# Kernel tuning notes

Hardware: AMD Instinct MI355X
Metric: run time of the kernel (lower is better)

The kernel has to match this reference:

```python
import jax, jax.numpy as jnp
import numpy as np

EPS = 1e-08


def setup_inputs() -> dict:
    key = jax.random.key(0)
    student_output = jax.random.normal(key, (8192, 1024), dtype=jnp.float32)
    return {"student_output": student_output}


def reference(student_output) -> jnp.ndarray:
    # F.normalize(p=2, dim=-1, eps=EPS): x / max(||x||_2, eps)
    x = student_output.astype(jnp.float32)
    norm = jnp.linalg.norm(x, axis=-1, keepdims=True)
    x = x / jnp.maximum(norm, EPS)

    n = x.shape[0]
    # full similarity matrix with diagonal masked to -1.0 (self-sim excluded)
    sim = x @ x.T  # [N, N]
    sim = jnp.where(jnp.eye(n, dtype=bool), jnp.float32(-1.0), sim)
    indices = jnp.argmax(sim, axis=1)  # nearest neighbor per row

    # torch.nn.PairwiseDistance(2, eps): ||x1 - x2 + eps||_2 along feature dim
    diff = x - x[indices] + EPS
    distances = jnp.sqrt(jnp.sum(diff * diff, axis=-1))

    return -jnp.mean(jnp.log(distances + EPS))
```

## Files before the change

### kernel.cpp

```cpp
#include <hip/hip_runtime.h>
#include <stdint.h>

#define N 8192
#define DIM 1024
#define EPSF 1e-8f
#define NBLK 32
#define NTRI 528

typedef __attribute__((ext_vector_type(4))) float f32x4;
typedef __attribute__((ext_vector_type(8))) short s16x8;

__device__ inline unsigned short f2bf(float f) {
  unsigned u = __float_as_uint(f);
  unsigned r = (u + 0x7FFFu + ((u >> 16) & 1u)) >> 16;
  return (unsigned short)r;
}

__device__ inline unsigned encf(float f) {
  unsigned u = __float_as_uint(f);
  return (u & 0x80000000u) ? ~u : (u | 0x80000000u);
}

#define XB_OFF   0
#define INV_OFF  16777216
#define KEY_OFF  16809984
#define PART_OFF 16875520

__global__ __launch_bounds__(256)
void k_norm(const float* __restrict__ x, unsigned short* __restrict__ xb,
            float* __restrict__ invn, unsigned long long* __restrict__ keys) {
  int row = blockIdx.x, t = threadIdx.x;
  const float4* xr = (const float4*)(x + (size_t)row * DIM);
  float4 v = xr[t];
  float ss = v.x * v.x + v.y * v.y + v.z * v.z + v.w * v.w;
#pragma unroll
  for (int o = 32; o > 0; o >>= 1) ss += __shfl_down(ss, o, 64);
  __shared__ float red[4];
  __shared__ float sinv;
  if ((t & 63) == 0) red[t >> 6] = ss;
  __syncthreads();
  if (t == 0) {
    float s = red[0] + red[1] + red[2] + red[3];
    float inv = 1.0f / fmaxf(sqrtf(s), EPSF);
    sinv = inv;
    invn[row] = inv;
    keys[row] = 0ull;
  }
  __syncthreads();
  float inv = sinv;
  ushort4 o4;
  o4.x = f2bf(v.x * inv);
  o4.y = f2bf(v.y * inv);
  o4.z = f2bf(v.z * inv);
  o4.w = f2bf(v.w * inv);
  ((ushort4*)(xb + (size_t)row * DIM))[t] = o4;
}

__global__ __launch_bounds__(512, 2)
void k_sim(const unsigned short* __restrict__ xb, unsigned long long* __restrict__ keys) {
  int b = blockIdx.x;
  int bi = (int)((65.0f - sqrtf(4225.0f - 8.0f * (float)b)) * 0.5f);
  while ((bi + 1) * (65 - (bi + 1)) / 2 <= b) ++bi;
  while (bi * (65 - bi) / 2 > b) --bi;
  int bj = bi + (b - bi * (65 - bi) / 2);

  __shared__ unsigned short sA[2][8192];
  __shared__ unsigned short sB[2][8192];

  const int t = threadIdx.x, lane = t & 63, wv = t >> 6;
  const int wr = wv >> 2, wc = wv & 3;
  const int hi = lane >> 4, lo = lane & 15;
  const int rowBase = bi * 256, colBase = bj * 256;

  const unsigned short* gA = xb + (size_t)rowBase * DIM;
  const unsigned short* gB = xb + (size_t)colBase * DIM;

  const int sg = (lane & 3) ^ ((lane >> 3) & 3);
  const int r0 = wv * 16 + (lane >> 2);
  const size_t so0 = (size_t)r0 * DIM + sg * 8;
  const size_t so1 = (size_t)(r0 + 128) * DIM + sg * 8;
  const int lb0 = wv * 512;
  const int lb1 = 4096 + wv * 512;

  const f32x4 fzero = {0.f, 0.f, 0.f, 0.f};
  f32x4 acc[8][4];
#pragma unroll
  for (int i = 0; i < 8; ++i)
#pragma unroll
    for (int j = 0; j < 4; ++j) acc[i][j] = fzero;

  const int sr8 = (hi ^ ((lo >> 1) & 3)) * 8;

  __builtin_amdgcn_global_load_lds((const __attribute__((address_space(1))) void*)(gA + so0),
                                   (__attribute__((address_space(3))) void*)(&sA[0][lb0]), 16, 0, 0);
  __builtin_amdgcn_global_load_lds((const __attribute__((address_space(1))) void*)(gA + so1),
                                   (__attribute__((address_space(3))) void*)(&sA[0][lb1]), 16, 0, 0);
  __builtin_amdgcn_global_load_lds((const __attribute__((address_space(1))) void*)(gB + so0),
                                   (__attribute__((address_space(3))) void*)(&sB[0][lb0]), 16, 0, 0);
  __builtin_amdgcn_global_load_lds((const __attribute__((address_space(1))) void*)(gB + so1),
                                   (__attribute__((address_space(3))) void*)(&sB[0][lb1]), 16, 0, 0);
  asm volatile("s_waitcnt vmcnt(0)" ::: "memory");
  __builtin_amdgcn_s_barrier();

  for (int kt = 0; kt < 32; ++kt) {
    const int cur = kt & 1, nxt = cur ^ 1;
    const size_t ko = (size_t)(kt + 1) * 32;
    s16x8 af[4], bf[4];

    if (kt < 31) {
      __builtin_amdgcn_global_load_lds((const __attribute__((address_space(1))) void*)(gA + so0 + ko),
                                       (__attribute__((address_space(3))) void*)(&sA[nxt][lb0]), 16, 0, 0);
      __builtin_amdgcn_global_load_lds((const __attribute__((address_space(1))) void*)(gA + so1 + ko),
                                       (__attribute__((address_space(3))) void*)(&sA[nxt][lb1]), 16, 0, 0);
    }
#pragma unroll
    for (int mi = 0; mi < 4; ++mi) {
      int r = wr * 128 + mi * 16 + lo;
      af[mi] = *(const s16x8*)(&sA[cur][r * 32 + sr8]);
    }
#pragma unroll
    for (int ni = 0; ni < 4; ++ni) {
      int r = wc * 64 + ni * 16 + lo;
      bf[ni] = *(const s16x8*)(&sB[cur][r * 32 + sr8]);
    }
    __builtin_amdgcn_s_barrier();
    __builtin_amdgcn_s_setprio(1);
#pragma unroll
    for (int mi = 0; mi < 4; ++mi)
#pragma unroll
      for (int ni = 0; ni < 4; ++ni)
        acc[mi][ni] = __builtin_amdgcn_mfma_f32_16x16x32_bf16(af[mi], bf[ni], acc[mi][ni], 0, 0, 0);
    __builtin_amdgcn_s_setprio(0);
    __builtin_amdgcn_s_barrier();

    if (kt < 31) {
      __builtin_amdgcn_global_load_lds((const __attribute__((address_space(1))) void*)(gB + so0 + ko),
                                       (__attribute__((address_space(3))) void*)(&sB[nxt][lb0]), 16, 0, 0);
      __builtin_amdgcn_global_load_lds((const __attribute__((address_space(1))) void*)(gB + so1 + ko),
                                       (__attribute__((address_space(3))) void*)(&sB[nxt][lb1]), 16, 0, 0);
    }
#pragma unroll
    for (int mi = 0; mi < 4; ++mi) {
      int r = wr * 128 + 64 + mi * 16 + lo;
      af[mi] = *(const s16x8*)(&sA[cur][r * 32 + sr8]);
    }
    __builtin_amdgcn_s_barrier();
    __builtin_amdgcn_s_setprio(1);
#pragma unroll
    for (int mi = 0; mi < 4; ++mi)
#pragma unroll
      for (int ni = 0; ni < 4; ++ni)
        acc[4 + mi][ni] = __builtin_amdgcn_mfma_f32_16x16x32_bf16(af[mi], bf[ni], acc[4 + mi][ni], 0, 0, 0);
    __builtin_amdgcn_s_setprio(0);
    asm volatile("s_waitcnt vmcnt(0)" ::: "memory");
    __builtin_amdgcn_s_barrier();
  }

#pragma unroll
  for (int am = 0; am < 8; ++am) {
#pragma unroll
    for (int reg = 0; reg < 4; ++reg) {
      int grow = rowBase + wr * 128 + am * 16 + hi * 4 + reg;
      float best = -10.0f;
      int bcol = 0;
#pragma unroll
      for (int ni = 0; ni < 4; ++ni) {
        int gcol = colBase + wc * 64 + ni * 16 + lo;
        float v = acc[am][ni][reg];
        v = (gcol == grow) ? -10.0f : v;
        if (v > best || (v == best && gcol < bcol)) { best = v; bcol = gcol; }
      }
#pragma unroll
      for (int m = 1; m < 16; m <<= 1) {
        float ov = __shfl_xor(best, m, 64);
        int oc = __shfl_xor(bcol, m, 64);
        if (ov > best || (ov == best && oc < bcol)) { best = ov; bcol = oc; }
      }
      if (lo == 0) {
        unsigned long long key = ((unsigned long long)encf(best) << 32) | (unsigned)(~bcol);
        atomicMax(&keys[grow], key);
      }
    }
  }

  if (bi != bj) {
#pragma unroll
    for (int ni = 0; ni < 4; ++ni) {
      int gcol = colBase + wc * 64 + ni * 16 + lo;
      float best = -10.0f;
      int brow = 0;
#pragma unroll
      for (int am = 0; am < 8; ++am)
#pragma unroll
        for (int reg = 0; reg < 4; ++reg) {
          int grow = rowBase + wr * 128 + am * 16 + hi * 4 + reg;
          float v = acc[am][ni][reg];
          if (v > best || (v == best && grow < brow)) { best = v; brow = grow; }
        }
#pragma unroll
      for (int m = 16; m < 64; m <<= 1) {
        float ov = __shfl_xor(best, m, 64);
        int oc = __shfl_xor(brow, m, 64);
        if (ov > best || (ov == best && oc < brow)) { best = ov; brow = oc; }
      }
      if (hi == 0) {
        unsigned long long key = ((unsigned long long)encf(best) << 32) | (unsigned)(~brow);
        atomicMax(&keys[gcol], key);
      }
    }
  }
}

__global__ __launch_bounds__(256)
void k_dist(const float* __restrict__ x, const float* __restrict__ invn,
            const unsigned long long* __restrict__ keys, float* __restrict__ part) {
  int row = blockIdx.x, t = threadIdx.x;
  unsigned long long key = keys[row];
  int nb = (int)(~(unsigned)key);
  float ia = invn[row], ib = invn[nb];
  float4 a = ((const float4*)(x + (size_t)row * DIM))[t];
  float4 b = ((const float4*)(x + (size_t)nb * DIM))[t];
  float d0 = a.x * ia - b.x * ib + EPSF;
  float d1 = a.y * ia - b.y * ib + EPSF;
  float d2 = a.z * ia - b.z * ib + EPSF;
  float d3 = a.w * ia - b.w * ib + EPSF;
  float ss = d0 * d0 + d1 * d1 + d2 * d2 + d3 * d3;
#pragma unroll
  for (int o = 32; o > 0; o >>= 1) ss += __shfl_down(ss, o, 64);
  __shared__ float red[4];
  if ((t & 63) == 0) red[t >> 6] = ss;
  __syncthreads();
  if (t == 0) {
    float s = red[0] + red[1] + red[2] + red[3];
    part[row] = logf(sqrtf(s) + EPSF);
  }
}

__global__ __launch_bounds__(1024)
void k_final(const float* __restrict__ part, float* __restrict__ out) {
  int t = threadIdx.x;
  float s = 0.0f;
#pragma unroll
  for (int i = 0; i < N / 1024; ++i) s += part[t + i * 1024];
#pragma unroll
  for (int o = 32; o > 0; o >>= 1) s += __shfl_down(s, o, 64);
  __shared__ float red[16];
  if ((t & 63) == 0) red[t >> 6] = s;
  __syncthreads();
  if (t == 0) {
    float tot = 0.0f;
#pragma unroll
    for (int i = 0; i < 16; ++i) tot += red[i];
    out[0] = -tot / (float)N;
  }
}

extern "C" void kernel_launch(void* const* d_in, const int* in_sizes, int n_in,
                              void* d_out, int out_size, void* d_ws, size_t ws_size,
                              hipStream_t stream) {
  const float* x = (const float*)d_in[0];
  float* out = (float*)d_out;
  char* ws = (char*)d_ws;
  unsigned short* xb = (unsigned short*)(ws + XB_OFF);
  float* invn = (float*)(ws + INV_OFF);
  unsigned long long* keys = (unsigned long long*)(ws + KEY_OFF);
  float* part = (float*)(ws + PART_OFF);

  k_norm<<<N, 256, 0, stream>>>(x, xb, invn, keys);
  k_sim<<<NTRI, 512, 0, stream>>>(xb, keys);
  k_dist<<<N, 256, 0, stream>>>(x, invn, keys, part);
  k_final<<<1, 1024, 0, stream>>>(part, out);
}
```

Before: 279.3 us.

## Use a four-stage LDS ring buffer with three tiles prefetched in k_sim

```diff
diff --git a/kernel.cpp b/kernel.cpp
--- a/kernel.cpp
+++ b/kernel.cpp
@@ -6,6 +6,7 @@
 #define EPSF 1e-8f
 #define NBLK 32
 #define NTRI 528
+#define NKT 32
 
 typedef __attribute__((ext_vector_type(4))) float f32x4;
 typedef __attribute__((ext_vector_type(8))) short s16x8;
@@ -58,15 +59,14 @@
 
 __global__ __launch_bounds__(512, 2)
 void k_sim(const unsigned short* __restrict__ xb, unsigned long long* __restrict__ keys) {
+  extern __shared__ unsigned short lds_us[];
+
   int b = blockIdx.x;
   int bi = (int)((65.0f - sqrtf(4225.0f - 8.0f * (float)b)) * 0.5f);
   while ((bi + 1) * (65 - (bi + 1)) / 2 <= b) ++bi;
   while (bi * (65 - bi) / 2 > b) --bi;
   int bj = bi + (b - bi * (65 - bi) / 2);
 
-  __shared__ unsigned short sA[2][8192];
-  __shared__ unsigned short sB[2][8192];
-
   const int t = threadIdx.x, lane = t & 63, wv = t >> 6;
   const int wr = wv >> 2, wc = wv & 3;
   const int hi = lane >> 4, lo = lane & 15;
@@ -76,11 +76,28 @@
   const unsigned short* gB = xb + (size_t)colBase * DIM;
 
   const int sg = (lane & 3) ^ ((lane >> 3) & 3);
-  const int r0 = wv * 16 + (lane >> 2);
-  const size_t so0 = (size_t)r0 * DIM + sg * 8;
-  const size_t so1 = (size_t)(r0 + 128) * DIM + sg * 8;
-  const int lb0 = wv * 512;
-  const int lb1 = 4096 + wv * 512;
+  const size_t soA0 = (size_t)(wv * 16 + (lane >> 2)) * DIM + sg * 8;
+  const size_t soA1 = soA0 + (size_t)128 * DIM;
+  const int ldsA0 = wv * 512;
+  const int ldsA1 = 4096 + wv * 512;
+
+#define STAGE_TILE(tt) do {                                                          \
+    const size_t ko_ = (size_t)(tt) * 32;                                            \
+    unsigned short* Ab_ = lds_us + ((tt) & 3) * 8192;                                \
+    unsigned short* Bb_ = lds_us + 32768 + ((tt) & 3) * 8192;                        \
+    __builtin_amdgcn_global_load_lds(                                                \
+        (const __attribute__((address_space(1))) void*)(gA + soA0 + ko_),            \
+        (__attribute__((address_space(3))) void*)(Ab_ + ldsA0), 16, 0, 0);           \
+    __builtin_amdgcn_global_load_lds(                                                \
+        (const __attribute__((address_space(1))) void*)(gA + soA1 + ko_),            \
+        (__attribute__((address_space(3))) void*)(Ab_ + ldsA1), 16, 0, 0);           \
+    __builtin_amdgcn_global_load_lds(                                                \
+        (const __attribute__((address_space(1))) void*)(gB + soA0 + ko_),            \
+        (__attribute__((address_space(3))) void*)(Bb_ + ldsA0), 16, 0, 0);           \
+    __builtin_amdgcn_global_load_lds(                                                \
+        (const __attribute__((address_space(1))) void*)(gB + soA1 + ko_),            \
+        (__attribute__((address_space(3))) void*)(Bb_ + ldsA1), 16, 0, 0);           \
+  } while (0)
 
   const f32x4 fzero = {0.f, 0.f, 0.f, 0.f};
   f32x4 acc[8][4];
@@ -89,72 +106,44 @@
 #pragma unroll
     for (int j = 0; j < 4; ++j) acc[i][j] = fzero;
 
-  const int sr8 = (hi ^ ((lo >> 1) & 3)) * 8;
-
-  __builtin_amdgcn_global_load_lds((const __attribute__((address_space(1))) void*)(gA + so0),
-                                   (__attribute__((address_space(3))) void*)(&sA[0][lb0]), 16, 0, 0);
-  __builtin_amdgcn_global_load_lds((const __attribute__((address_space(1))) void*)(gA + so1),
-                                   (__attribute__((address_space(3))) void*)(&sA[0][lb1]), 16, 0, 0);
-  __builtin_amdgcn_global_load_lds((const __attribute__((address_space(1))) void*)(gB + so0),
-                                   (__attribute__((address_space(3))) void*)(&sB[0][lb0]), 16, 0, 0);
-  __builtin_amdgcn_global_load_lds((const __attribute__((address_space(1))) void*)(gB + so1),
-                                   (__attribute__((address_space(3))) void*)(&sB[0][lb1]), 16, 0, 0);
-  asm volatile("s_waitcnt vmcnt(0)" ::: "memory");
-  __builtin_amdgcn_s_barrier();
-
-  for (int kt = 0; kt < 32; ++kt) {
-    const int cur = kt & 1, nxt = cur ^ 1;
-    const size_t ko = (size_t)(kt + 1) * 32;
-    s16x8 af[4], bf[4];
-
-    if (kt < 31) {
-      __builtin_amdgcn_global_load_lds((const __attribute__((address_space(1))) void*)(gA + so0 + ko),
-                                       (__attribute__((address_space(3))) void*)(&sA[nxt][lb0]), 16, 0, 0);
-      __builtin_amdgcn_global_load_lds((const __attribute__((address_space(1))) void*)(gA + so1 + ko),
-                                       (__attribute__((address_space(3))) void*)(&sA[nxt][lb1]), 16, 0, 0);
-    }
-#pragma unroll
-    for (int mi = 0; mi < 4; ++mi) {
+  const int chux = (hi ^ ((lo >> 1) & 3)) * 8;
+
+  STAGE_TILE(0);
+  STAGE_TILE(1);
+  STAGE_TILE(2);
+  asm volatile("s_waitcnt vmcnt(8)" ::: "memory");
+  asm volatile("s_barrier" ::: "memory");
+
+  for (int kt = 0; kt < NKT; ++kt) {
+    if (kt < NKT - 3) STAGE_TILE(kt + 3);
+
+    const unsigned short* Ab = lds_us + (kt & 3) * 8192;
+    const unsigned short* Bb = lds_us + 32768 + (kt & 3) * 8192;
+    s16x8 af[8], bfr[4];
+#pragma unroll
+    for (int mi = 0; mi < 8; ++mi) {
       int r = wr * 128 + mi * 16 + lo;
-      af[mi] = *(const s16x8*)(&sA[cur][r * 32 + sr8]);
+      af[mi] = *(const s16x8*)(Ab + r * 32 + chux);
     }
 #pragma unroll
     for (int ni = 0; ni < 4; ++ni) {
       int r = wc * 64 + ni * 16 + lo;
-      bf[ni] = *(const s16x8*)(&sB[cur][r * 32 + sr8]);
-    }
-    __builtin_amdgcn_s_barrier();
+      bfr[ni] = *(const s16x8*)(Bb + r * 32 + chux);
+    }
+
     __builtin_amdgcn_s_setprio(1);
 #pragma unroll
-    for (int mi = 0; mi < 4; ++mi)
+    for (int mi = 0; mi < 8; ++mi)
 #pragma unroll
       for (int ni = 0; ni < 4; ++ni)
-        acc[mi][ni] = __builtin_amdgcn_mfma_f32_16x16x32_bf16(af[mi], bf[ni], acc[mi][ni], 0, 0, 0);
+        acc[mi][ni] = __builtin_amdgcn_mfma_f32_16x16x32_bf16(af[mi], bfr[ni], acc[mi][ni], 0, 0, 0);
     __builtin_amdgcn_s_setprio(0);
-    __builtin_amdgcn_s_barrier();
-
-    if (kt < 31) {
-      __builtin_amdgcn_global_load_lds((const __attribute__((address_space(1))) void*)(gB + so0 + ko),
-                                       (__attribute__((address_space(3))) void*)(&sB[nxt][lb0]), 16, 0, 0);
-      __builtin_amdgcn_global_load_lds((const __attribute__((address_space(1))) void*)(gB + so1 + ko),
-                                       (__attribute__((address_space(3))) void*)(&sB[nxt][lb1]), 16, 0, 0);
-    }
-#pragma unroll
-    for (int mi = 0; mi < 4; ++mi) {
-      int r = wr * 128 + 64 + mi * 16 + lo;
-      af[mi] = *(const s16x8*)(&sA[cur][r * 32 + sr8]);
-    }
-    __builtin_amdgcn_s_barrier();
-    __builtin_amdgcn_s_setprio(1);
-#pragma unroll
-    for (int mi = 0; mi < 4; ++mi)
-#pragma unroll
-      for (int ni = 0; ni < 4; ++ni)
-        acc[4 + mi][ni] = __builtin_amdgcn_mfma_f32_16x16x32_bf16(af[mi], bf[ni], acc[4 + mi][ni], 0, 0, 0);
-    __builtin_amdgcn_s_setprio(0);
-    asm volatile("s_waitcnt vmcnt(0)" ::: "memory");
-    __builtin_amdgcn_s_barrier();
-  }
+
+    if (kt < NKT - 3) asm volatile("s_waitcnt vmcnt(8)" ::: "memory");
+    else              asm volatile("s_waitcnt vmcnt(0)" ::: "memory");
+    asm volatile("s_barrier" ::: "memory");
+  }
+#undef STAGE_TILE
 
 #pragma unroll
   for (int am = 0; am < 8; ++am) {
@@ -266,8 +255,11 @@
   unsigned long long* keys = (unsigned long long*)(ws + KEY_OFF);
   float* part = (float*)(ws + PART_OFF);
 
+  (void)hipFuncSetAttribute((const void*)k_sim,
+                            hipFuncAttributeMaxDynamicSharedMemorySize, 131072);
+
   k_norm<<<N, 256, 0, stream>>>(x, xb, invn, keys);
-  k_sim<<<NTRI, 512, 0, stream>>>(xb, keys);
+  k_sim<<<NTRI, 512, 131072, stream>>>(xb, keys);
   k_dist<<<N, 256, 0, stream>>>(x, invn, keys, part);
   k_final<<<1, 1024, 0, stream>>>(part, out);
 }
```

New measurement: 239.9 us. 14.1% less time.
